# Kernel optimization log

Measured on AMD Instinct MI355X. Metric: run time of the kernel, lower is better.

The kernel has to match this reference:

```python
import jax, jax.numpy as jnp
import numpy as np

NUM_NODES = 50000
NUM_EDGES = 800000
NUM_FEATURES = 128
HIDDEN = 128
NUM_GRAPHS = 256


def gcn_conv(x, W, b, src, dst, num_nodes):
    """PyG GCNConv: add self-loops, symmetric deg normalization, scatter-add, bias."""
    h = x @ W  # [N, H]
    # add self-loops
    loop = jnp.arange(num_nodes, dtype=src.dtype)
    src_f = jnp.concatenate([src, loop])
    dst_f = jnp.concatenate([dst, loop])
    # degree of destination nodes (includes self-loops)
    deg = jax.ops.segment_sum(jnp.ones_like(dst_f, dtype=h.dtype), dst_f,
                              num_segments=num_nodes)
    dinv = jnp.where(deg > 0, jax.lax.rsqrt(deg), 0.0)
    norm = dinv[src_f] * dinv[dst_f]  # [E+N]
    msg = h[src_f] * norm[:, None]    # gather + scale
    out = jax.ops.segment_sum(msg, dst_f, num_segments=num_nodes)
    return out + b


def global_mean_pool(x, batch, num_graphs):
    s = jax.ops.segment_sum(x, batch, num_segments=num_graphs)
    cnt = jax.ops.segment_sum(jnp.ones((x.shape[0],), dtype=x.dtype), batch,
                              num_segments=num_graphs)
    return s / jnp.maximum(cnt, 1.0)[:, None]


def setup_inputs() -> dict:
    key = jax.random.key(0)
    ks = jax.random.split(key, 8)
    x = jax.random.normal(ks[0], (NUM_NODES, NUM_FEATURES), dtype=jnp.float32)
    edge_index = jax.random.randint(ks[1], (2, NUM_EDGES), 0, NUM_NODES, dtype=jnp.int64)
    batch = jax.random.randint(ks[2], (NUM_NODES,), 0, NUM_GRAPHS, dtype=jnp.int64)
    # glorot-ish init for weights
    s1 = 1.0 / np.sqrt(NUM_FEATURES)
    s2 = 1.0 / np.sqrt(HIDDEN)
    W1 = jax.random.normal(ks[3], (NUM_FEATURES, HIDDEN), dtype=jnp.float32) * s1
    b1 = jnp.zeros((HIDDEN,), dtype=jnp.float32)
    W2 = jax.random.normal(ks[4], (HIDDEN, HIDDEN), dtype=jnp.float32) * s2
    b2 = jnp.zeros((HIDDEN,), dtype=jnp.float32)
    lin_W = jax.random.normal(ks[5], (HIDDEN, 1), dtype=jnp.float32) * s2
    lin_b = jnp.zeros((1,), dtype=jnp.float32)
    return {"x": x, "edge_index": edge_index, "batch": batch,
            "W1": W1, "b1": b1, "W2": W2, "b2": b2,
            "lin_W": lin_W, "lin_b": lin_b}


def reference(x, edge_index, batch, W1, b1, W2, b2, lin_W, lin_b):
    src, dst = edge_index[0], edge_index[1]
    n = x.shape[0]
    h = jax.nn.relu(gcn_conv(x, W1, b1, src, dst, n))
    h = jax.nn.relu(gcn_conv(h, W2, b2, src, dst, n))
    g = global_mean_pool(h, batch, NUM_GRAPHS)  # [G, H]
    return g @ lin_W + lin_b                    # [G, 1]
```

## Files before the change

kernel.cpp:

```cpp
#include <hip/hip_runtime.h>

#define NFEAT 128
#define NPART 64
#define CAP   64

typedef unsigned int uint;
typedef __attribute__((ext_vector_type(8))) short short8v;
typedef __attribute__((ext_vector_type(8))) unsigned short ushort8v;
typedef __attribute__((ext_vector_type(4))) float floatx4;

__device__ inline float bf2f(unsigned short u) {
    return __uint_as_float(((uint)u) << 16);
}
__device__ inline unsigned short f2bf(float f) {
    uint u = __float_as_uint(f);
    return (unsigned short)((u + 0x7fffu + ((u >> 16) & 1u)) >> 16);
}

__global__ __launch_bounds__(256) void zero_kernel(int4* __restrict__ p, int n4) {
    int i = blockIdx.x * 256 + threadIdx.x;
    int stride = gridDim.x * 256;
    int4 z = make_int4(0, 0, 0, 0);
    for (; i < n4; i += stride) p[i] = z;
}

__global__ void prep_kernel(const int* __restrict__ src, const int* __restrict__ dst,
                            const int* __restrict__ batch,
                            const float* __restrict__ W1, const float* __restrict__ W2,
                            int* __restrict__ cnt, unsigned short* __restrict__ csr,
                            unsigned short* __restrict__ wt, float* __restrict__ gcntp,
                            int E, int N) {
    if (blockIdx.x < 4096) {
        const int shard = blockIdx.x & 7;
        const int blk = blockIdx.x >> 3;
        const int span = (N + 7) >> 3;
        const int lo = shard * span;
        const int hi = min(N, lo + span);
        const int stride = 512 * 256;
        const int base = blk * 256 + (int)threadIdx.x;
        for (int eb = base; eb < E; eb += 7 * stride) {
            int dv[7], sv[7];
#pragma unroll
            for (int t = 0; t < 7; ++t) {
                int e = eb + t * stride;
                dv[t] = (e < E) ? dst[e] : -1;
                sv[t] = (e < E) ? src[e] : 0;
            }
#pragma unroll
            for (int t = 0; t < 7; ++t) {
                int d = dv[t];
                if (d >= lo && d < hi) {
                    int pos = atomicAdd(&cnt[d], 1);
                    if (pos < CAP) csr[d * CAP + pos] = (unsigned short)sv[t];
                }
            }
        }
    } else {
        const int idx = (blockIdx.x - 4096) * 256 + threadIdx.x;
        {
            const float* W = (idx < 16384) ? W1 : W2;
            int i = idx & 16383;
            int k = i >> 7, n = i & 127;
            float v = W[k * 128 + n];
            unsigned short h = f2bf(v);
            unsigned short l = f2bf(v - bf2f(h));
            unsigned short* base = wt + (idx < 16384 ? 0 : 2) * 16384;
            base[n * 128 + k] = h;
            base[16384 + n * 128 + k] = l;
        }
        for (int v = idx; v < N; v += 128 * 256)
            atomicAdd(&gcntp[(v & (NPART - 1)) * 256 + batch[v]], 1.0f);
    }
}

__global__ __launch_bounds__(256) void gemm1_mfma_kernel(const float* __restrict__ X,
                                                         const unsigned short* __restrict__ wt,
                                                         const int* __restrict__ cnt,
                                                         unsigned short* __restrict__ out,
                                                         int nrows) {
    __shared__ unsigned short xs_hi[64][72], xs_lo[64][72];
    const int tid = threadIdx.x;
    const int w = tid >> 6, lane = tid & 63;
    const int nl = lane & 15, kg = lane >> 4;
    const int row0 = blockIdx.x * 64;

    floatx4 acc[8];
#pragma unroll
    for (int nt = 0; nt < 8; ++nt) acc[nt] = (floatx4){0.f, 0.f, 0.f, 0.f};

    for (int p = 0; p < 2; ++p) {
        __syncthreads();
        for (int idx = tid; idx < 64 * 16; idx += 256) {
            int r = idx >> 4, q = idx & 15;
            float4 v = make_float4(0.f, 0.f, 0.f, 0.f);
            if (row0 + r < nrows)
                v = ((const float4*)(X + (size_t)(row0 + r) * NFEAT + p * 64))[q];
            ushort4 h, l;
            h.x = f2bf(v.x); l.x = f2bf(v.x - bf2f(h.x));
            h.y = f2bf(v.y); l.y = f2bf(v.y - bf2f(h.y));
            h.z = f2bf(v.z); l.z = f2bf(v.z - bf2f(h.z));
            h.w = f2bf(v.w); l.w = f2bf(v.w - bf2f(h.w));
            *(ushort4*)&xs_hi[r][q * 4] = h;
            *(ushort4*)&xs_lo[r][q * 4] = l;
        }
        __syncthreads();
#pragma unroll
        for (int kc = 0; kc < 2; ++kc) {
            const int k8 = kc * 32 + kg * 8;
            const int kgl = p * 64 + k8;
            short8v ah = *(const short8v*)&xs_hi[w * 16 + nl][k8];
            short8v al = *(const short8v*)&xs_lo[w * 16 + nl][k8];
#pragma unroll
            for (int nt = 0; nt < 8; ++nt) {
                short8v bh = *(const short8v*)(wt + (size_t)(nt * 16 + nl) * 128 + kgl);
                short8v bl = *(const short8v*)(wt + 16384 + (size_t)(nt * 16 + nl) * 128 + kgl);
                acc[nt] = __builtin_amdgcn_mfma_f32_16x16x32_bf16(ah, bh, acc[nt], 0, 0, 0);
                acc[nt] = __builtin_amdgcn_mfma_f32_16x16x32_bf16(al, bh, acc[nt], 0, 0, 0);
                acc[nt] = __builtin_amdgcn_mfma_f32_16x16x32_bf16(ah, bl, acc[nt], 0, 0, 0);
            }
        }
    }
    const int rbase = row0 + w * 16 + kg * 4;
#pragma unroll
    for (int reg = 0; reg < 4; ++reg) {
        int grow = rbase + reg;
        if (grow < nrows) {
            float dv = rsqrtf((float)(cnt[grow] + 1));
#pragma unroll
            for (int nt = 0; nt < 8; ++nt)
                out[(size_t)grow * NFEAT + nt * 16 + nl] = f2bf(acc[nt][reg] * dv);
        }
    }
}

__global__ __launch_bounds__(256) void gemm2_mfma_kernel(const unsigned short* __restrict__ X,
                                                         const unsigned short* __restrict__ wt,
                                                         const int* __restrict__ cnt,
                                                         unsigned short* __restrict__ out,
                                                         int nrows) {
    __shared__ unsigned short xs[64][72];
    const int tid = threadIdx.x;
    const int w = tid >> 6, lane = tid & 63;
    const int nl = lane & 15, kg = lane >> 4;
    const int row0 = blockIdx.x * 64;

    floatx4 acc[8];
#pragma unroll
    for (int nt = 0; nt < 8; ++nt) acc[nt] = (floatx4){0.f, 0.f, 0.f, 0.f};

    for (int p = 0; p < 2; ++p) {
        __syncthreads();
        for (int idx = tid; idx < 64 * 8; idx += 256) {
            int r = idx >> 3, q = idx & 7;
            short8v v = {0, 0, 0, 0, 0, 0, 0, 0};
            if (row0 + r < nrows)
                v = *(const short8v*)(X + (size_t)(row0 + r) * NFEAT + p * 64 + q * 8);
            *(short8v*)&xs[r][q * 8] = v;
        }
        __syncthreads();
#pragma unroll
        for (int kc = 0; kc < 2; ++kc) {
            const int k8 = kc * 32 + kg * 8;
            const int kgl = p * 64 + k8;
            short8v a = *(const short8v*)&xs[w * 16 + nl][k8];
#pragma unroll
            for (int nt = 0; nt < 8; ++nt) {
                short8v bh = *(const short8v*)(wt + (size_t)(nt * 16 + nl) * 128 + kgl);
                short8v bl = *(const short8v*)(wt + 16384 + (size_t)(nt * 16 + nl) * 128 + kgl);
                acc[nt] = __builtin_amdgcn_mfma_f32_16x16x32_bf16(a, bh, acc[nt], 0, 0, 0);
                acc[nt] = __builtin_amdgcn_mfma_f32_16x16x32_bf16(a, bl, acc[nt], 0, 0, 0);
            }
        }
    }
    const int rbase = row0 + w * 16 + kg * 4;
#pragma unroll
    for (int reg = 0; reg < 4; ++reg) {
        int grow = rbase + reg;
        if (grow < nrows) {
            float dv = rsqrtf((float)(cnt[grow] + 1));
#pragma unroll
            for (int nt = 0; nt < 8; ++nt)
                out[(size_t)grow * NFEAT + nt * 16 + nl] = f2bf(acc[nt][reg] * dv);
        }
    }
}

__device__ inline void agg_gather8(const ushort8v* __restrict__ hp8,
                                   const unsigned short* __restrict__ csr,
                                   int v, int d, int ep, int q, float acc[8]) {
    const int s = v * CAP;
    if (ep == 0) {
        ushort8v r = hp8[(size_t)v * 16 + q];
#pragma unroll
        for (int k = 0; k < 8; ++k) acc[k] += bf2f(r[k]);
    }
    int i = 0;
    for (; i + 16 <= d; i += 16) {
        int u[4];
#pragma unroll
        for (int j = 0; j < 4; ++j) u[j] = csr[s + i + 4 * j + ep];
        ushort8v a[4];
#pragma unroll
        for (int j = 0; j < 4; ++j) a[j] = hp8[(size_t)u[j] * 16 + q];
#pragma unroll
        for (int j = 0; j < 4; ++j)
#pragma unroll
            for (int k = 0; k < 8; ++k) acc[k] += bf2f(a[j][k]);
    }
    if (i < d) {
        int u[4];
#pragma unroll
        for (int j = 0; j < 4; ++j) {
            int e = i + 4 * j + ep;
            u[j] = csr[s + (e < d ? e : d - 1)];
        }
        ushort8v a[4];
#pragma unroll
        for (int j = 0; j < 4; ++j) a[j] = hp8[(size_t)u[j] * 16 + q];
#pragma unroll
        for (int j = 0; j < 4; ++j) {
            if (i + 4 * j + ep < d) {
#pragma unroll
                for (int k = 0; k < 8; ++k) acc[k] += bf2f(a[j][k]);
            }
        }
    }
#pragma unroll
    for (int k = 0; k < 8; ++k) {
        acc[k] += __shfl_xor(acc[k], 16);
        acc[k] += __shfl_xor(acc[k], 32);
    }
}

__global__ __launch_bounds__(256) void agg_relu_kernel(const ushort8v* __restrict__ hp8,
                                                       const int* __restrict__ cnt,
                                                       const unsigned short* __restrict__ csr,
                                                       const float* __restrict__ bias,
                                                       unsigned short* __restrict__ out,
                                                       int N, int npw) {
    const int wgl = (blockIdx.x * 256 + threadIdx.x) >> 6;
    const int lane = threadIdx.x & 63;
    const int ep = lane >> 4;
    const int q = lane & 15;
    float4 bb0 = *(const float4*)(bias + q * 8);
    float4 bb1 = *(const float4*)(bias + q * 8 + 4);
    const int v0 = wgl * npw;
    const int v1 = min(N, v0 + npw);
    for (int v = v0; v < v1; ++v) {
        int d = cnt[v];
        float acc[8] = {0, 0, 0, 0, 0, 0, 0, 0};
        agg_gather8(hp8, csr, v, d, ep, q, acc);
        if (ep == 0) {
            const float dv = rsqrtf((float)(d + 1));
            ushort8v o;
            o[0] = f2bf(fmaxf(fmaf(acc[0], dv, bb0.x), 0.f));
            o[1] = f2bf(fmaxf(fmaf(acc[1], dv, bb0.y), 0.f));
            o[2] = f2bf(fmaxf(fmaf(acc[2], dv, bb0.z), 0.f));
            o[3] = f2bf(fmaxf(fmaf(acc[3], dv, bb0.w), 0.f));
            o[4] = f2bf(fmaxf(fmaf(acc[4], dv, bb1.x), 0.f));
            o[5] = f2bf(fmaxf(fmaf(acc[5], dv, bb1.y), 0.f));
            o[6] = f2bf(fmaxf(fmaf(acc[6], dv, bb1.z), 0.f));
            o[7] = f2bf(fmaxf(fmaf(acc[7], dv, bb1.w), 0.f));
            *(ushort8v*)(out + (size_t)v * NFEAT + q * 8) = o;
        }
    }
}

__global__ __launch_bounds__(256) void agg_pool_kernel(const ushort8v* __restrict__ hp8,
                                                       const int* __restrict__ cnt,
                                                       const unsigned short* __restrict__ csr,
                                                       const float* __restrict__ bias,
                                                       const float* __restrict__ linW,
                                                       const int* __restrict__ batch,
                                                       float* __restrict__ gpart,
                                                       int N, int npw) {
    const int wgl = (blockIdx.x * 256 + threadIdx.x) >> 6;
    const int lane = threadIdx.x & 63;
    const int ep = lane >> 4;
    const int q = lane & 15;
    float4 bb0 = *(const float4*)(bias + q * 8);
    float4 bb1 = *(const float4*)(bias + q * 8 + 4);
    float4 lw0 = *(const float4*)(linW + q * 8);
    float4 lw1 = *(const float4*)(linW + q * 8 + 4);
    const int v0 = wgl * npw;
    const int v1 = min(N, v0 + npw);
    for (int v = v0; v < v1; ++v) {
        int d = cnt[v];
        float acc[8] = {0, 0, 0, 0, 0, 0, 0, 0};
        agg_gather8(hp8, csr, v, d, ep, q, acc);
        const float dv = rsqrtf((float)(d + 1));
        float sc = fmaxf(fmaf(acc[0], dv, bb0.x), 0.f) * lw0.x
                 + fmaxf(fmaf(acc[1], dv, bb0.y), 0.f) * lw0.y
                 + fmaxf(fmaf(acc[2], dv, bb0.z), 0.f) * lw0.z
                 + fmaxf(fmaf(acc[3], dv, bb0.w), 0.f) * lw0.w
                 + fmaxf(fmaf(acc[4], dv, bb1.x), 0.f) * lw1.x
                 + fmaxf(fmaf(acc[5], dv, bb1.y), 0.f) * lw1.y
                 + fmaxf(fmaf(acc[6], dv, bb1.z), 0.f) * lw1.z
                 + fmaxf(fmaf(acc[7], dv, bb1.w), 0.f) * lw1.w;
        sc += __shfl_xor(sc, 1);
        sc += __shfl_xor(sc, 2);
        sc += __shfl_xor(sc, 4);
        sc += __shfl_xor(sc, 8);
        if (lane == 0) atomicAdd(&gpart[(v & (NPART - 1)) * 256 + batch[v]], sc);
    }
}

__global__ void finalize_kernel(const float* __restrict__ gpart, const float* __restrict__ gcntp,
                                const float* __restrict__ linb, float* __restrict__ out, int G) {
    int g = threadIdx.x;
    if (g < G) {
        float s = 0.f, c = 0.f;
        for (int p = 0; p < NPART; ++p) {
            s += gpart[p * 256 + g];
            c += gcntp[p * 256 + g];
        }
        out[g] = s / fmaxf(c, 1.0f) + linb[0];
    }
}

extern "C" void kernel_launch(void* const* d_in, const int* in_sizes, int n_in,
                              void* d_out, int out_size, void* d_ws, size_t ws_size,
                              hipStream_t stream) {
    const float* x    = (const float*)d_in[0];
    const int*   eidx = (const int*)d_in[1];
    const int*   batch= (const int*)d_in[2];
    const float* W1   = (const float*)d_in[3];
    const float* b1   = (const float*)d_in[4];
    const float* W2   = (const float*)d_in[5];
    const float* b2   = (const float*)d_in[6];
    const float* linW = (const float*)d_in[7];
    const float* linb = (const float*)d_in[8];
    float* out = (float*)d_out;

    const int N = in_sizes[0] / NFEAT;
    const int E = in_sizes[1] / 2;
    const int G = out_size;
    const int* src = eidx;
    const int* dst = eidx + E;

    char* p = (char*)d_ws;
    unsigned short* hpBf  = (unsigned short*)p; p += (size_t)N * NFEAT * sizeof(unsigned short);
    unsigned short* h1Bf  = (unsigned short*)p; p += (size_t)N * NFEAT * sizeof(unsigned short);
    unsigned short* hp2Bf = (unsigned short*)p; p += (size_t)N * NFEAT * sizeof(unsigned short);
    unsigned short* csr   = (unsigned short*)p; p += (size_t)N * CAP * sizeof(unsigned short);
    unsigned short* wt    = (unsigned short*)p; p += (size_t)4 * 16384 * sizeof(unsigned short);
    int*   cnt   = (int*)p;   p += (size_t)N * sizeof(int);
    float* gpart = (float*)p; p += (size_t)NPART * 256 * sizeof(float);
    float* gcntp = (float*)p; p += (size_t)NPART * 256 * sizeof(float);
    (void)ws_size; (void)n_in;

    const int nz4 = (int)(((size_t)N + 2 * NPART * 256 + 3) / 4);
    zero_kernel<<<256, 256, 0, stream>>>((int4*)cnt, nz4);

    prep_kernel<<<4224, 256, 0, stream>>>(src, dst, batch, W1, W2, cnt, csr, wt, gcntp, E, N);

    const int NWAVE = 2048 * 4;
    const int npw = (N + NWAVE - 1) / NWAVE;

    gemm1_mfma_kernel<<<(N + 63) / 64, 256, 0, stream>>>(x, wt, cnt, hpBf, N);
    agg_relu_kernel<<<2048, 256, 0, stream>>>((const ushort8v*)hpBf, cnt, csr,
                                              b1, h1Bf, N, npw);
    gemm2_mfma_kernel<<<(N + 63) / 64, 256, 0, stream>>>(h1Bf, wt + 2 * 16384, cnt, hp2Bf, N);
    agg_pool_kernel<<<2048, 256, 0, stream>>>((const ushort8v*)hp2Bf, cnt, csr,
                                              b2, linW, batch, gpart, N, npw);
    finalize_kernel<<<1, 256, 0, stream>>>(gpart, gcntp, linb, out, G);
}
```

Measured before the change: 185.8 us.

## Fuse finalize into pooling kernel, use LDS histogram for graph counts, simplify edge scatter

The separate finalize launch is removed: the last block of agg_pool, detected with an atomic done counter after a threadfence, reduces the partial sums and graph counts and writes the output. Graph node counts are now built per block in an LDS histogram and written as a non-atomic partial row, replacing global float atomics. The edge-binning loop drops its 7-way manual unroll in favour of a simple strided loop using nontemporal loads, with src loaded only for edges that fall in the shard. This saves one kernel launch and cuts global atomic traffic, at the cost of a grid-wide completion counter and a serial tail reduction inside the last block.

```diff
diff --git a/kernel.cpp b/kernel.cpp
--- a/kernel.cpp
+++ b/kernel.cpp
@@ -2,6 +2,7 @@
 
 #define NFEAT 128
 #define NPART 64
+#define NAUX  128
 #define CAP   64
 
 typedef unsigned int uint;
@@ -37,26 +38,18 @@
         const int lo = shard * span;
         const int hi = min(N, lo + span);
         const int stride = 512 * 256;
-        const int base = blk * 256 + (int)threadIdx.x;
-        for (int eb = base; eb < E; eb += 7 * stride) {
-            int dv[7], sv[7];
-#pragma unroll
-            for (int t = 0; t < 7; ++t) {
-                int e = eb + t * stride;
-                dv[t] = (e < E) ? dst[e] : -1;
-                sv[t] = (e < E) ? src[e] : 0;
+        for (int e = blk * 256 + (int)threadIdx.x; e < E; e += stride) {
+            int d = __builtin_nontemporal_load(dst + e);
+            if (d >= lo && d < hi) {
+                int pos = atomicAdd(&cnt[d], 1);
+                if (pos < CAP)
+                    csr[d * CAP + pos] = (unsigned short)__builtin_nontemporal_load(src + e);
             }
-#pragma unroll
-            for (int t = 0; t < 7; ++t) {
-                int d = dv[t];
-                if (d >= lo && d < hi) {
-                    int pos = atomicAdd(&cnt[d], 1);
-                    if (pos < CAP) csr[d * CAP + pos] = (unsigned short)sv[t];
-                }
-            }
         }
     } else {
-        const int idx = (blockIdx.x - 4096) * 256 + threadIdx.x;
+        const int ab = blockIdx.x - 4096;
+        const int tid = threadIdx.x;
+        const int idx = ab * 256 + tid;
         {
             const float* W = (idx < 16384) ? W1 : W2;
             int i = idx & 16383;
@@ -68,8 +61,15 @@
             base[n * 128 + k] = h;
             base[16384 + n * 128 + k] = l;
         }
-        for (int v = idx; v < N; v += 128 * 256)
-            atomicAdd(&gcntp[(v & (NPART - 1)) * 256 + batch[v]], 1.0f);
+        __shared__ int hist[256];
+        hist[tid] = 0;
+        __syncthreads();
+        const int per = (N + NAUX - 1) / NAUX;
+        const int lo2 = ab * per;
+        const int hi2 = min(N, lo2 + per);
+        for (int v = lo2 + tid; v < hi2; v += 256) atomicAdd(&hist[batch[v]], 1);
+        __syncthreads();
+        gcntp[ab * 256 + tid] = (float)hist[tid];
     }
 }
 
@@ -273,48 +273,58 @@
                                                        const float* __restrict__ linW,
                                                        const int* __restrict__ batch,
                                                        float* __restrict__ gpart,
-                                                       int N, int npw) {
-    const int wgl = (blockIdx.x * 256 + threadIdx.x) >> 6;
+                                                       const float* __restrict__ gcntp,
+                                                       const float* __restrict__ linb,
+                                                       int* __restrict__ done,
+                                                       float* __restrict__ out,
+                                                       int N, int npw, int G) {
     const int lane = threadIdx.x & 63;
     const int ep = lane >> 4;
     const int q = lane & 15;
-    float4 bb0 = *(const float4*)(bias + q * 8);
-    float4 bb1 = *(const float4*)(bias + q * 8 + 4);
-    float4 lw0 = *(const float4*)(linW + q * 8);
-    float4 lw1 = *(const float4*)(linW + q * 8 + 4);
-    const int v0 = wgl * npw;
-    const int v1 = min(N, v0 + npw);
-    for (int v = v0; v < v1; ++v) {
-        int d = cnt[v];
-        float acc[8] = {0, 0, 0, 0, 0, 0, 0, 0};
-        agg_gather8(hp8, csr, v, d, ep, q, acc);
-        const float dv = rsqrtf((float)(d + 1));
-        float sc = fmaxf(fmaf(acc[0], dv, bb0.x), 0.f) * lw0.x
-                 + fmaxf(fmaf(acc[1], dv, bb0.y), 0.f) * lw0.y
-                 + fmaxf(fmaf(acc[2], dv, bb0.z), 0.f) * lw0.z
-                 + fmaxf(fmaf(acc[3], dv, bb0.w), 0.f) * lw0.w
-                 + fmaxf(fmaf(acc[4], dv, bb1.x), 0.f) * lw1.x
-                 + fmaxf(fmaf(acc[5], dv, bb1.y), 0.f) * lw1.y
-                 + fmaxf(fmaf(acc[6], dv, bb1.z), 0.f) * lw1.z
-                 + fmaxf(fmaf(acc[7], dv, bb1.w), 0.f) * lw1.w;
-        sc += __shfl_xor(sc, 1);
-        sc += __shfl_xor(sc, 2);
-        sc += __shfl_xor(sc, 4);
-        sc += __shfl_xor(sc, 8);
-        if (lane == 0) atomicAdd(&gpart[(v & (NPART - 1)) * 256 + batch[v]], sc);
-    }
-}
-
-__global__ void finalize_kernel(const float* __restrict__ gpart, const float* __restrict__ gcntp,
-                                const float* __restrict__ linb, float* __restrict__ out, int G) {
-    int g = threadIdx.x;
-    if (g < G) {
-        float s = 0.f, c = 0.f;
-        for (int p = 0; p < NPART; ++p) {
-            s += gpart[p * 256 + g];
-            c += gcntp[p * 256 + g];
-        }
-        out[g] = s / fmaxf(c, 1.0f) + linb[0];
+    {
+        const int wgl = (blockIdx.x * 256 + threadIdx.x) >> 6;
+        float4 bb0 = *(const float4*)(bias + q * 8);
+        float4 bb1 = *(const float4*)(bias + q * 8 + 4);
+        float4 lw0 = *(const float4*)(linW + q * 8);
+        float4 lw1 = *(const float4*)(linW + q * 8 + 4);
+        const int v0 = wgl * npw;
+        const int v1 = min(N, v0 + npw);
+        for (int v = v0; v < v1; ++v) {
+            int d = cnt[v];
+            float acc[8] = {0, 0, 0, 0, 0, 0, 0, 0};
+            agg_gather8(hp8, csr, v, d, ep, q, acc);
+            const float dv = rsqrtf((float)(d + 1));
+            float sc = fmaxf(fmaf(acc[0], dv, bb0.x), 0.f) * lw0.x
+                     + fmaxf(fmaf(acc[1], dv, bb0.y), 0.f) * lw0.y
+                     + fmaxf(fmaf(acc[2], dv, bb0.z), 0.f) * lw0.z
+                     + fmaxf(fmaf(acc[3], dv, bb0.w), 0.f) * lw0.w
+                     + fmaxf(fmaf(acc[4], dv, bb1.x), 0.f) * lw1.x
+                     + fmaxf(fmaf(acc[5], dv, bb1.y), 0.f) * lw1.y
+                     + fmaxf(fmaf(acc[6], dv, bb1.z), 0.f) * lw1.z
+                     + fmaxf(fmaf(acc[7], dv, bb1.w), 0.f) * lw1.w;
+            sc += __shfl_xor(sc, 1);
+            sc += __shfl_xor(sc, 2);
+            sc += __shfl_xor(sc, 4);
+            sc += __shfl_xor(sc, 8);
+            if (lane == 0) atomicAdd(&gpart[(v & (NPART - 1)) * 256 + batch[v]], sc);
+        }
+    }
+    __threadfence();
+    __shared__ int lastFlag;
+    if (threadIdx.x == 0)
+        lastFlag = (atomicAdd(done, 1) == (int)gridDim.x - 1) ? 1 : 0;
+    __syncthreads();
+    if (lastFlag) {
+        int g = threadIdx.x;
+        if (g < G) {
+            float s = 0.f;
+            for (int pp = 0; pp < NPART; ++pp)
+                s += __hip_atomic_load(&gpart[pp * 256 + g], __ATOMIC_RELAXED,
+                                       __HIP_MEMORY_SCOPE_AGENT);
+            float c = 0.f;
+            for (int b = 0; b < NAUX; ++b) c += gcntp[b * 256 + g];
+            out[g] = s / fmaxf(c, 1.0f) + linb[0];
+        }
     }
 }
 
@@ -346,13 +356,15 @@
     unsigned short* wt    = (unsigned short*)p; p += (size_t)4 * 16384 * sizeof(unsigned short);
     int*   cnt   = (int*)p;   p += (size_t)N * sizeof(int);
     float* gpart = (float*)p; p += (size_t)NPART * 256 * sizeof(float);
-    float* gcntp = (float*)p; p += (size_t)NPART * 256 * sizeof(float);
+    int*   done  = (int*)p;   p += 4 * sizeof(int);
+    float* gcntp = (float*)p; p += (size_t)NAUX * 256 * sizeof(float);
     (void)ws_size; (void)n_in;
 
-    const int nz4 = (int)(((size_t)N + 2 * NPART * 256 + 3) / 4);
+    const int nz4 = (int)(((size_t)N * 4 + (size_t)NPART * 256 * 4 + 16) / 16);
     zero_kernel<<<256, 256, 0, stream>>>((int4*)cnt, nz4);
 
-    prep_kernel<<<4224, 256, 0, stream>>>(src, dst, batch, W1, W2, cnt, csr, wt, gcntp, E, N);
+    prep_kernel<<<4096 + NAUX, 256, 0, stream>>>(src, dst, batch, W1, W2, cnt, csr, wt,
+                                                 gcntp, E, N);
 
     const int NWAVE = 2048 * 4;
     const int npw = (N + NWAVE - 1) / NWAVE;
@@ -362,6 +374,6 @@
                                               b1, h1Bf, N, npw);
     gemm2_mfma_kernel<<<(N + 63) / 64, 256, 0, stream>>>(h1Bf, wt + 2 * 16384, cnt, hp2Bf, N);
     agg_pool_kernel<<<2048, 256, 0, stream>>>((const ushort8v*)hp2Bf, cnt, csr,
-                                              b2, linW, batch, gpart, N, npw);
-    finalize_kernel<<<1, 256, 0, stream>>>(gpart, gcntp, linb, out, G);
-}
+                                              b2, linW, batch, gpart, gcntp, linb,
+                                              done, out, N, npw, G);
+}
```

After: 351.5 us. 89.2% more time.
